# Performance work log

Hardware: AMD Instinct MI355X
Metric: run time of the kernel (lower is better)

## Reference

```python
import jax, jax.numpy as jnp
import numpy as np

DILATIONS = (1, 2, 4, 8)
K = 3  # kernel_size
B, H, W, C = 16, 128, 128, 64
HID = 256
OUT = 64  # == C, so residual path is taken


def _depthwise(x, w, dilation):
    # x: [B,H,W,C], w: [K,K,1,C] (HWIO depthwise kernel)
    pad = dilation * (K // 2)
    return jax.lax.conv_general_dilated(
        x, w,
        window_strides=(1, 1),
        padding=[(pad, pad), (pad, pad)],
        rhs_dilation=(dilation, dilation),
        dimension_numbers=('NHWC', 'HWIO', 'NHWC'),
        feature_group_count=C,
    )


def setup_inputs() -> dict:
    key = jax.random.key(0)
    k_x, k_cw, k_w1, k_b1, k_w2, k_b2 = jax.random.split(key, 6)
    in_feat = C * (1 + len(DILATIONS))  # 320
    x = jax.random.normal(k_x, (B, H, W, C), jnp.float32)
    # depthwise kernels, one [K,K,1,C] per dilation, stacked
    conv_w = jax.random.normal(k_cw, (len(DILATIONS), K, K, 1, C), jnp.float32) * (1.0 / np.sqrt(K * K).astype(np.float32))
    W1 = jax.random.normal(k_w1, (in_feat, HID), jnp.float32) * np.float32(1.0 / np.sqrt(in_feat))
    b1 = jax.random.normal(k_b1, (HID,), jnp.float32) * 0.01
    W2 = jax.random.normal(k_w2, (HID, OUT), jnp.float32) * np.float32(1.0 / np.sqrt(HID))
    b2 = jax.random.normal(k_b2, (OUT,), jnp.float32) * 0.01
    return {"x": x, "conv_w": conv_w, "W1": W1, "b1": b1, "W2": W2, "b2": b2}


def reference(x, conv_w, W1, b1, W2, b2):
    # 1) Perception: multiscale depthwise dilated convs (same-padding per dilation)
    perceptions = [_depthwise(x, conv_w[i], d) for i, d in enumerate(DILATIONS)]
    upd_in = jnp.concatenate([x] + perceptions, axis=-1)  # [B,H,W,5C]
    # 2) Update MLP: Linear -> Dropout(eval: identity) -> GELU(exact erf) -> Linear
    h = jax.nn.gelu(upd_in @ W1 + b1, approximate=False)  # [B,H,W,HID]
    delta = h @ W2 + b2  # [B,H,W,OUT]
    # 3) out_channels == channels and (eval mode or fire_rate==1.0): plain residual
    return x + delta
```

## Files before the change

### kernel.cpp

```cpp
#include <hip/hip_runtime.h>
#include <hip/hip_fp16.h>
#include <cstdint>

#define B_   16
#define H_   128
#define W_   128
#define C_   64
#define HID_ 256
#define XELEMS (B_ * H_ * W_ * C_)

typedef _Float16 __attribute__((ext_vector_type(2))) half2v;
typedef _Float16 __attribute__((ext_vector_type(8))) half8v;
typedef __attribute__((ext_vector_type(4))) float f32x4;
typedef unsigned short ushort_t;

#define W1S_OFF 0
#define W2S_OFF 81920
#define CWH_OFF 98304
#define XH_OFF  100608
#define FEAT_OFF (XH_OFF + XELEMS)
#define FEAT_HALVES (4096ull * 16384ull)
#define WS_NEED_FULL (2ull * (FEAT_OFF + FEAT_HALVES))

__device__ __forceinline__ int hs(int row, int col) {
  return row * 256 + (((col >> 3) ^ (row & 7)) << 3) + (col & 7);
}

__device__ __forceinline__ float fast_gelu(float h) {
  float u = h * fmaf(h * h, 0.10293921f, 2.30211813f);
  float e = exp2f(-u);
  return h * __builtin_amdgcn_rcpf(1.0f + e);
}

__device__ __forceinline__ uint32_t fast_gelu_pk(float h0, float h1) {
  half2v h = __builtin_bit_cast(half2v, __builtin_amdgcn_cvt_pkrtz(h0, h1));
  const half2v c1 = {(_Float16)0.10293921f, (_Float16)0.10293921f};
  const half2v c0 = {(_Float16)2.30211813f, (_Float16)2.30211813f};
  half2v u = h * (c0 + h * h * c1);
  __half2 e = h2exp2(__hneg2(__builtin_bit_cast(__half2, u)));
  const __half2 one = __half2{(__half)1.0f, (__half)1.0f};
  __half2 s = h2rcp(__hadd2(one, e));
  __half2 g = __hmul2(__builtin_bit_cast(__half2, h), s);
  return __builtin_bit_cast(uint32_t, g);
}

__device__ __forceinline__ void stage16(const _Float16* g, const ushort_t* l) {
  __builtin_amdgcn_global_load_lds(
      (const __attribute__((address_space(1))) void*)g,
      (__attribute__((address_space(3))) void*)l, 16, 0, 0);
}

__device__ __forceinline__ half2v bch(uint32_t u) {
  return __builtin_bit_cast(half2v, u);
}

__global__ void prep_kernel(const float* __restrict__ x,
                            const float* __restrict__ W1,
                            const float* __restrict__ W2,
                            const float* __restrict__ cw,
                            _Float16* __restrict__ wsb) {
  if (blockIdx.x < 393) {
    int t = blockIdx.x * 256 + threadIdx.x;
    if (t < 81920) {
      int j = t & 7, lane = (t >> 3) & 63, n16 = (t >> 9) & 15, ks = t >> 13;
      int k = ks * 32 + (lane >> 4) * 8 + j;
      int n = n16 * 16 + (lane & 15);
      wsb[W1S_OFF + t] = (_Float16)W1[k * 256 + n];
    } else if (t < 98304) {
      int t2 = t - 81920;
      int j = t2 & 7, lane = (t2 >> 3) & 63, n16 = (t2 >> 9) & 3, ks = t2 >> 11;
      int k = ks * 32 + (lane >> 4) * 8 + j;
      int n = n16 * 16 + (lane & 15);
      wsb[W2S_OFF + t2] = (_Float16)W2[k * 64 + n];
    } else if (t < 98304 + 2304) {
      int t3 = t - 98304;
      wsb[CWH_OFF + t3] = (_Float16)cw[t3];
    }
  } else {
    int i = ((blockIdx.x - 393) * 256 + threadIdx.x) * 8;
    const float4 a = *(const float4*)&x[i];
    const float4 b = *(const float4*)&x[i + 4];
    half8v o = {(_Float16)a.x, (_Float16)a.y, (_Float16)a.z, (_Float16)a.w,
                (_Float16)b.x, (_Float16)b.y, (_Float16)b.z, (_Float16)b.w};
    *(half8v*)&wsb[XH_OFF + i] = o;
  }
}

template <int DIL, int DDI>
__device__ void conv_boundary(const _Float16* __restrict__ xhb,
                              const _Float16* __restrict__ cwh,
                              _Float16* __restrict__ ft,
                              int tid, int tileX, int tileY) {
  const int quad = tid & 15;
  const int p0   = tid >> 4;
  const int ksq  = quad >> 3;
  const int c32  = (quad & 7) * 4;

  half2v w01[9], w23[9];
#pragma unroll
  for (int t = 0; t < 9; ++t) {
    uint2 wr = *(const uint2*)&cwh[(DDI * 9 + t) * C_ + quad * 4];
    w01[t] = bch(wr.x);
    w23[t] = bch(wr.y);
  }
#pragma unroll
  for (int i = 0; i < 4; ++i) {
    const int p  = i * 16 + p0;
    const int y0 = tileY + (p >> 3), x0 = tileX + (p & 7);
    half2v a01 = {0, 0}, a23 = {0, 0};
#pragma unroll
    for (int ky = 0; ky < 3; ++ky) {
      const int yy = y0 + (ky - 1) * DIL;
#pragma unroll
      for (int kx = 0; kx < 3; ++kx) {
        const int xx = x0 + (kx - 1) * DIL;
        uint2 vv = {0u, 0u};
        if ((unsigned)yy < (unsigned)H_ && (unsigned)xx < (unsigned)W_)
          vv = *(const uint2*)&xhb[(yy * W_ + xx) * C_ + quad * 4];
        const int t = ky * 3 + kx;
        a01 += bch(vv.x) * w01[t];
        a23 += bch(vv.y) * w23[t];
      }
    }
    uint2 pk;
    pk.x = __builtin_bit_cast(uint32_t, a01);
    pk.y = __builtin_bit_cast(uint32_t, a23);
    *(uint2*)&ft[(DDI * 2 + ksq) * 2048 + p * 32 + c32] = pk;
  }
}

template <int DIL, int DDI>
__global__ __launch_bounds__(256)
void conv_lds_kernel(const _Float16* __restrict__ xh,
                     const _Float16* __restrict__ cwh,
                     _Float16* __restrict__ feat) {
  constexpr int R = 8 + 2 * DIL;
  __shared__ __align__(16) ushort_t lds[R * 1024];

  const int tid   = threadIdx.x;
  const int tileX = blockIdx.x * 8;
  const int tileY = blockIdx.y * 8;
  const int batch = blockIdx.z;
  const _Float16* xhb = xh + (size_t)batch * (H_ * W_ * C_);
  _Float16* ft =
      feat + ((size_t)((batch * 16 + blockIdx.y) * 16 + blockIdx.x)) * 16384;

  const bool interior = (tileX >= 8) && (tileX <= W_ - 16) &&
                        (tileY >= 8) && (tileY <= H_ - 16);
  if (!interior) {
    conv_boundary<DIL, DDI>(xhb, cwh, ft, tid, tileX, tileY);
    return;
  }

  const int lane = tid & 63;
  const int wv   = tid >> 6;
  const int quad = tid & 15;
  const int p0   = tid >> 4;
  const int ksq  = quad >> 3;
  const int c32  = (quad & 7) * 4;

  {
    const int x0 = tileX - DIL, y0 = tileY - DIL;
    for (int s = wv; s < 2 * R; s += 4) {
      const int row = s >> 1, half = s & 1;
      const _Float16* g = &xhb[((y0 + row) * W_ + x0 + half * 8 + (lane >> 3)) * C_ +
                               (lane & 7) * 8];
      stage16(g, &lds[row * 1024 + half * 512]);
    }
  }

  half2v w01[9], w23[9];
#pragma unroll
  for (int t = 0; t < 9; ++t) {
    uint2 wr = *(const uint2*)&cwh[(DDI * 9 + t) * C_ + quad * 4];
    w01[t] = bch(wr.x);
    w23[t] = bch(wr.y);
  }

  __syncthreads();

#pragma unroll
  for (int i = 0; i < 4; ++i) {
    const int p  = i * 16 + p0;
    const int py = p >> 3, px = p & 7;
    uint2 tv[9];
#pragma unroll
    for (int ky = 0; ky < 3; ++ky)
#pragma unroll
      for (int kx = 0; kx < 3; ++kx)
        tv[ky * 3 + kx] = *(const uint2*)
            &lds[(py + ky * DIL) * 1024 + (px + kx * DIL) * 64 + quad * 4];
    half2v a01 = {0, 0}, a23 = {0, 0};
#pragma unroll
    for (int t = 0; t < 9; ++t) {
      a01 += bch(tv[t].x) * w01[t];
      a23 += bch(tv[t].y) * w23[t];
    }
    uint2 pk;
    pk.x = __builtin_bit_cast(uint32_t, a01);
    pk.y = __builtin_bit_cast(uint32_t, a23);
    *(uint2*)&ft[(DDI * 2 + ksq) * 2048 + p * 32 + c32] = pk;
  }
}

__global__ __launch_bounds__(256)
void conv_d8_kernel(const _Float16* __restrict__ xh,
                    const _Float16* __restrict__ cwh,
                    _Float16* __restrict__ feat) {
  const int tid   = threadIdx.x;
  const int tileX = blockIdx.x * 8;
  const int tileY = blockIdx.y * 8;
  const int batch = blockIdx.z;
  const _Float16* xhb = xh + (size_t)batch * (H_ * W_ * C_);
  _Float16* ft =
      feat + ((size_t)((batch * 16 + blockIdx.y) * 16 + blockIdx.x)) * 16384;

  const int c8 = tid & 7;
  const int p0 = tid >> 3;
  const int ksq = c8 >> 2;
  const int cof = (c8 & 3) * 8;

  uint4 wv4[9];
#pragma unroll
  for (int t = 0; t < 9; ++t)
    wv4[t] = *(const uint4*)&cwh[(3 * 9 + t) * C_ + c8 * 8];

  const bool interior = (tileX >= 8) && (tileX <= W_ - 16) &&
                        (tileY >= 8) && (tileY <= H_ - 16);

#pragma unroll
  for (int i = 0; i < 2; ++i) {
    const int p  = i * 32 + p0;
    const int y0 = tileY + (p >> 3), x0 = tileX + (p & 7);
    uint4 v[9];
    if (interior) {
#pragma unroll
      for (int ky = 0; ky < 3; ++ky)
#pragma unroll
        for (int kx = 0; kx < 3; ++kx)
          v[ky * 3 + kx] = *(const uint4*)
              &xhb[((y0 + (ky - 1) * 8) * W_ + x0 + (kx - 1) * 8) * C_ + c8 * 8];
    } else {
#pragma unroll
      for (int ky = 0; ky < 3; ++ky)
#pragma unroll
        for (int kx = 0; kx < 3; ++kx) {
          const int yy = y0 + (ky - 1) * 8;
          const int xx = x0 + (kx - 1) * 8;
          uint4 vv = {0u, 0u, 0u, 0u};
          if ((unsigned)yy < (unsigned)H_ && (unsigned)xx < (unsigned)W_)
            vv = *(const uint4*)&xhb[(yy * W_ + xx) * C_ + c8 * 8];
          v[ky * 3 + kx] = vv;
        }
    }
    half2v a0 = {0, 0}, a1 = {0, 0}, a2 = {0, 0}, a3 = {0, 0};
#pragma unroll
    for (int t = 0; t < 9; ++t) {
      a0 += bch(v[t].x) * bch(wv4[t].x);
      a1 += bch(v[t].y) * bch(wv4[t].y);
      a2 += bch(v[t].z) * bch(wv4[t].z);
      a3 += bch(v[t].w) * bch(wv4[t].w);
    }
    uint4 pk;
    pk.x = __builtin_bit_cast(uint32_t, a0);
    pk.y = __builtin_bit_cast(uint32_t, a1);
    pk.z = __builtin_bit_cast(uint32_t, a2);
    pk.w = __builtin_bit_cast(uint32_t, a3);
    *(uint4*)&ft[(3 * 2 + ksq) * 2048 + p * 32 + cof] = pk;
  }
}

__global__ __launch_bounds__(256, 4)
void mlp_kernel(const _Float16* __restrict__ xh,
                const _Float16* __restrict__ feat,
                const float* __restrict__ b1,
                const float* __restrict__ b2,
                const _Float16* __restrict__ w1s,
                const _Float16* __restrict__ w2s,
                float* __restrict__ out) {
  __shared__ __align__(16) ushort_t smem[64 * 256];

  const int tid   = threadIdx.x;
  const int tileX = blockIdx.x * 8;
  const int tileY = blockIdx.y * 8;
  const int batch = blockIdx.z;
  const _Float16* xhb = xh + (size_t)batch * (H_ * W_ * C_);
  const _Float16* ftb =
      feat + ((size_t)((batch * 16 + blockIdx.y) * 16 + blockIdx.x)) * 16384;

  const int lane = tid & 63;
  const int wv   = tid >> 6;
  const int lr   = lane & 15;
  const int lg   = lane >> 4;
  const int n0   = wv * 64;

  const half8v* w1v = (const half8v*)w1s;

  half8v xf[4][2];
#pragma unroll
  for (int pi = 0; pi < 4; ++pi) {
    const int p  = pi * 16 + lr;
    const int gp = (tileY + (p >> 3)) * W_ + tileX + (p & 7);
#pragma unroll
    for (int ks = 0; ks < 2; ++ks)
      xf[pi][ks] = *(const half8v*)&xhb[gp * C_ + ks * 32 + lg * 8];
  }

  {
    const _Float16* src0 = &ftb[(wv * 16 + lr) * 32 + lg * 8];
#pragma unroll
    for (int s = 0; s < 8; ++s)
      stage16(src0 + s * 2048, &smem[(s * 4 + wv) * 512]);
  }

  f32x4 acc[4][4];
#pragma unroll
  for (int hi = 0; hi < 4; ++hi)
#pragma unroll
    for (int pi = 0; pi < 4; ++pi) acc[hi][pi] = 0;

#pragma unroll
  for (int ks = 0; ks < 2; ++ks) {
    half8v wf[4];
#pragma unroll
    for (int hi = 0; hi < 4; ++hi)
      wf[hi] = w1v[(ks * 16 + wv * 4 + hi) * 64 + lane];
#pragma unroll
    for (int hi = 0; hi < 4; ++hi)
#pragma unroll
      for (int pi = 0; pi < 4; ++pi)
        acc[hi][pi] = __builtin_amdgcn_mfma_f32_16x16x32_f16(
            wf[hi], xf[pi][ks], acc[hi][pi], 0, 0, 0);
  }

  __syncthreads();

#define LOAD_W(WB, S)                                                         \
  _Pragma("unroll") for (int hi = 0; hi < 4; ++hi)                            \
      WB[hi] = w1v[((S) * 16 + wv * 4 + hi) * 64 + lane];
#define LOAD_F(FB, S)                                                         \
  _Pragma("unroll") for (int pi = 0; pi < 4; ++pi)                            \
      FB[pi] = *(const half8v*)&smem[(((S) - 2) * 4 + pi) * 512 + lane * 8];
#define MFMA16(WB, FB)                                                        \
  _Pragma("unroll") for (int hi = 0; hi < 4; ++hi)                            \
      _Pragma("unroll") for (int pi = 0; pi < 4; ++pi)                        \
      acc[hi][pi] = __builtin_amdgcn_mfma_f32_16x16x32_f16(                   \
          WB[hi], FB[pi], acc[hi][pi], 0, 0, 0);

  {
    half8v wfA[4], wfB[4], fA[4];
    LOAD_W(wfA, 2);
    LOAD_F(fA, 2); LOAD_W(wfB, 3); MFMA16(wfA, fA);
    LOAD_F(fA, 3); LOAD_W(wfA, 4); MFMA16(wfB, fA);
    LOAD_F(fA, 4); LOAD_W(wfB, 5); MFMA16(wfA, fA);
    LOAD_F(fA, 5); LOAD_W(wfA, 6); MFMA16(wfB, fA);
    LOAD_F(fA, 6); LOAD_W(wfB, 7); MFMA16(wfA, fA);
    LOAD_F(fA, 7); LOAD_W(wfA, 8); MFMA16(wfB, fA);
    LOAD_F(fA, 8); LOAD_W(wfB, 9); MFMA16(wfA, fA);
    LOAD_F(fA, 9);                 MFMA16(wfB, fA);
  }

  float4 bias1[4];
#pragma unroll
  for (int hi = 0; hi < 4; ++hi)
    bias1[hi] = *(const float4*)&b1[n0 + hi * 16 + lg * 4];

  __syncthreads();

#pragma unroll
  for (int hi = 0; hi < 4; ++hi) {
#pragma unroll
    for (int pi = 0; pi < 4; ++pi) {
      uint2 pk;
      pk.x = fast_gelu_pk(acc[hi][pi][0] + bias1[hi][0],
                          acc[hi][pi][1] + bias1[hi][1]);
      pk.y = fast_gelu_pk(acc[hi][pi][2] + bias1[hi][2],
                          acc[hi][pi][3] + bias1[hi][3]);
      *(uint2*)&smem[hs(pi * 16 + lr, n0 + hi * 16 + lg * 4)] = pk;
    }
  }
  __syncthreads();

  const int m0 = wv * 16;
  f32x4 acc2[4];
#pragma unroll
  for (int ni = 0; ni < 4; ++ni) acc2[ni] = 0;

  const half8v* w2v = (const half8v*)w2s;
#pragma unroll 2
  for (int ks = 0; ks < 8; ++ks) {
    half8v a2 = *(const half8v*)&smem[hs(m0 + lr, ks * 32 + lg * 8)];
#pragma unroll
    for (int ni = 0; ni < 4; ++ni) {
      half8v bfr = w2v[(ks * 4 + ni) * 64 + lane];
      acc2[ni] = __builtin_amdgcn_mfma_f32_16x16x32_f16(a2, bfr, acc2[ni],
                                                        0, 0, 0);
    }
  }

#pragma unroll
  for (int ni = 0; ni < 4; ++ni) {
    const int col  = ni * 16 + lr;
    const float bias = b2[col];
#pragma unroll
    for (int q = 0; q < 4; ++q) {
      const int row = m0 + lg * 4 + q;
      const int py = row >> 3, px = row & 7;
      const size_t idx =
          ((size_t)(batch * H_ + tileY + py) * W_ + (tileX + px)) * C_ + col;
      out[idx] = (float)xh[idx] + acc2[ni][q] + bias;
    }
  }
#undef LOAD_W
#undef LOAD_F
#undef MFMA16
}

template <bool BOUND>
__device__ __forceinline__ void conv_phase_f32(const float* __restrict__ xb,
                                               const _Float16* __restrict__ cwh,
                                               ushort_t* __restrict__ feat,
                                               int tid, int tileX, int tileY) {
  const int quad = tid & 15;
  const int p0   = tid >> 4;
#pragma unroll
  for (int dd = 0; dd < 4; ++dd) {
    const int dil = 1 << dd;
    half2v w01[9], w23[9];
#pragma unroll
    for (int t = 0; t < 9; ++t) {
      uint2 wr = *(const uint2*)&cwh[(dd * 9 + t) * C_ + quad * 4];
      w01[t] = bch(wr.x);
      w23[t] = bch(wr.y);
    }
#pragma unroll
    for (int i = 0; i < 4; ++i) {
      const int p  = i * 16 + p0;
      const int y0 = tileY + (p >> 3), x0 = tileX + (p & 7);
      half2v a01 = {0, 0}, a23 = {0, 0};
#pragma unroll
      for (int ky = 0; ky < 3; ++ky) {
        const int yy = y0 + (ky - 1) * dil;
        if (BOUND && (unsigned)yy >= (unsigned)H_) continue;
#pragma unroll
        for (int kx = 0; kx < 3; ++kx) {
          const int xx = x0 + (kx - 1) * dil;
          if (BOUND && (unsigned)xx >= (unsigned)W_) continue;
          const int t = ky * 3 + kx;
          const float4 xv = *(const float4*)&xb[(yy * W_ + xx) * C_ + quad * 4];
          half2v xl = {(_Float16)xv.x, (_Float16)xv.y};
          half2v xh2 = {(_Float16)xv.z, (_Float16)xv.w};
          a01 += xl * w01[t];
          a23 += xh2 * w23[t];
        }
      }
      uint2 pk;
      pk.x = __builtin_bit_cast(uint32_t, a01);
      pk.y = __builtin_bit_cast(uint32_t, a23);
      *(uint2*)&feat[hs(p, dd * 64 + quad * 4)] = pk;
    }
  }
}

__global__ __launch_bounds__(256, 4)
void nca_fused_fp32(const float* __restrict__ x,
                    const _Float16* __restrict__ cwh,
                    const float* __restrict__ b1,
                    const float* __restrict__ b2,
                    const _Float16* __restrict__ w1s,
                    const _Float16* __restrict__ w2s,
                    float* __restrict__ out) {
  __shared__ __align__(16) ushort_t smem[64 * 256];

  const int tid   = threadIdx.x;
  const int tileX = blockIdx.x * 8;
  const int tileY = blockIdx.y * 8;
  const int batch = blockIdx.z;
  const float* xb = x + (size_t)batch * (H_ * W_ * C_);

  const int lane = tid & 63;
  const int wv   = tid >> 6;
  const int lr   = lane & 15;
  const int lg   = lane >> 4;
  const int n0   = wv * 64;

  half8v xf[4][2];
#pragma unroll
  for (int pi = 0; pi < 4; ++pi) {
    const int p  = pi * 16 + lr;
    const int gp = (tileY + (p >> 3)) * W_ + tileX + (p & 7);
#pragma unroll
    for (int ks = 0; ks < 2; ++ks) {
      const float* bp = &xb[gp * C_ + ks * 32 + lg * 8];
      float4 u = *(const float4*)bp, v = *(const float4*)(bp + 4);
      half8v s = {(_Float16)u.x, (_Float16)u.y, (_Float16)u.z, (_Float16)u.w,
                  (_Float16)v.x, (_Float16)v.y, (_Float16)v.z, (_Float16)v.w};
      xf[pi][ks] = s;
    }
  }

  const bool interior = (tileX >= 8) && (tileX <= W_ - 16) &&
                        (tileY >= 8) && (tileY <= H_ - 16);
  if (interior)
    conv_phase_f32<false>(xb, cwh, smem, tid, tileX, tileY);
  else
    conv_phase_f32<true>(xb, cwh, smem, tid, tileX, tileY);
  __syncthreads();

  f32x4 acc[4][4];
#pragma unroll
  for (int hi = 0; hi < 4; ++hi)
#pragma unroll
    for (int pi = 0; pi < 4; ++pi) acc[hi][pi] = 0;

  const half8v* w1v = (const half8v*)w1s;
#pragma unroll
  for (int ks = 0; ks < 2; ++ks) {
    half8v wf[4];
#pragma unroll
    for (int hi = 0; hi < 4; ++hi)
      wf[hi] = w1v[(ks * 16 + wv * 4 + hi) * 64 + lane];
#pragma unroll
    for (int hi = 0; hi < 4; ++hi)
#pragma unroll
      for (int pi = 0; pi < 4; ++pi)
        acc[hi][pi] = __builtin_amdgcn_mfma_f32_16x16x32_f16(
            wf[hi], xf[pi][ks], acc[hi][pi], 0, 0, 0);
  }
  for (int ks = 2; ks < 10; ++ks) {
    half8v ff[4], wf[4];
#pragma unroll
    for (int pi = 0; pi < 4; ++pi)
      ff[pi] = *(const half8v*)&smem[hs(pi * 16 + lr, (ks - 2) * 32 + lg * 8)];
#pragma unroll
    for (int hi = 0; hi < 4; ++hi)
      wf[hi] = w1v[(ks * 16 + wv * 4 + hi) * 64 + lane];
#pragma unroll
    for (int hi = 0; hi < 4; ++hi)
#pragma unroll
      for (int pi = 0; pi < 4; ++pi)
        acc[hi][pi] = __builtin_amdgcn_mfma_f32_16x16x32_f16(
            wf[hi], ff[pi], acc[hi][pi], 0, 0, 0);
  }

  float4 bias1[4];
#pragma unroll
  for (int hi = 0; hi < 4; ++hi)
    bias1[hi] = *(const float4*)&b1[n0 + hi * 16 + lg * 4];

  __syncthreads();

#pragma unroll
  for (int hi = 0; hi < 4; ++hi) {
#pragma unroll
    for (int pi = 0; pi < 4; ++pi) {
      _Float16 g[4];
#pragma unroll
      for (int q = 0; q < 4; ++q)
        g[q] = (_Float16)fast_gelu(acc[hi][pi][q] + bias1[hi][q]);
      half2v g01 = {g[0], g[1]}, g23 = {g[2], g[3]};
      uint2 pk;
      pk.x = __builtin_bit_cast(uint32_t, g01);
      pk.y = __builtin_bit_cast(uint32_t, g23);
      *(uint2*)&smem[hs(pi * 16 + lr, n0 + hi * 16 + lg * 4)] = pk;
    }
  }
  __syncthreads();

  const int m0 = wv * 16;
  f32x4 acc2[4];
#pragma unroll
  for (int ni = 0; ni < 4; ++ni) acc2[ni] = 0;

  const half8v* w2v = (const half8v*)w2s;
  for (int ks = 0; ks < 8; ++ks) {
    half8v a2 = *(const half8v*)&smem[hs(m0 + lr, ks * 32 + lg * 8)];
#pragma unroll
    for (int ni = 0; ni < 4; ++ni) {
      half8v bfr = w2v[(ks * 4 + ni) * 64 + lane];
      acc2[ni] = __builtin_amdgcn_mfma_f32_16x16x32_f16(a2, bfr, acc2[ni],
                                                        0, 0, 0);
    }
  }

#pragma unroll
  for (int ni = 0; ni < 4; ++ni) {
    const int col  = ni * 16 + lr;
    const float bias = b2[col];
#pragma unroll
    for (int q = 0; q < 4; ++q) {
      const int row = m0 + lg * 4 + q;
      const int py = row >> 3, px = row & 7;
      const size_t idx =
          ((size_t)(batch * H_ + tileY + py) * W_ + (tileX + px)) * C_ + col;
      out[idx] = x[idx] + acc2[ni][q] + bias;
    }
  }
}

extern "C" void kernel_launch(void* const* d_in, const int* in_sizes, int n_in,
                              void* d_out, int out_size, void* d_ws,
                              size_t ws_size, hipStream_t stream) {
  const float* x  = (const float*)d_in[0];
  const float* cw = (const float*)d_in[1];
  const float* W1 = (const float*)d_in[2];
  const float* b1 = (const float*)d_in[3];
  const float* W2 = (const float*)d_in[4];
  const float* b2 = (const float*)d_in[5];
  float* out = (float*)d_out;

  _Float16* wsb  = (_Float16*)d_ws;
  _Float16* w1s  = wsb + W1S_OFF;
  _Float16* w2s  = wsb + W2S_OFF;
  _Float16* cwh  = wsb + CWH_OFF;
  _Float16* xh   = wsb + XH_OFF;
  _Float16* feat = wsb + FEAT_OFF;

  if (ws_size >= (size_t)WS_NEED_FULL) {
    prep_kernel<<<393 + XELEMS / 8 / 256, 256, 0, stream>>>(x, W1, W2, cw, wsb);
    dim3 g16(W_ / 8, H_ / 8, B_);
    conv_lds_kernel<1, 0><<<g16, 256, 0, stream>>>(xh, cwh, feat);
    conv_lds_kernel<2, 1><<<g16, 256, 0, stream>>>(xh, cwh, feat);
    conv_lds_kernel<4, 2><<<g16, 256, 0, stream>>>(xh, cwh, feat);
    conv_d8_kernel<<<g16, 256, 0, stream>>>(xh, cwh, feat);
    mlp_kernel<<<g16, 256, 0, stream>>>(xh, feat, b1, b2, w1s, w2s, out);
  } else {
    prep_kernel<<<393, 256, 0, stream>>>(x, W1, W2, cw, wsb);
    dim3 grid(W_ / 8, H_ / 8, B_);
    nca_fused_fp32<<<grid, 256, 0, stream>>>(x, cwh, b1, b2, w1s, w2s, out);
  }
}
```

Baseline: 198.4 us.

## Merge four per-dilation conv launches into one kernel indexed by blockIdx.z

Replaces the three templated LDS conv kernels and the separate dilation-8 kernel with one conv_all_kernel. It uses a grid four times deeper in z and picks the dilation at runtime from blockIdx.z. This removes three kernel launches and their serialization tails, so all dilations run at the same time. The dilation-8 path also issues all 18 global loads before any compute, with asm barriers to keep them grouped. In exchange, dilation becomes a runtime value rather than a compile-time constant, LDS is sized for the worst case (16 rows, 32 KB), and occupancy is bounded by launch_bounds(256,2).

After: 181.7 us, median of 2. -8.4%, faster.

```diff
diff --git a/kernel.cpp b/kernel.cpp
--- a/kernel.cpp
+++ b/kernel.cpp
@@ -86,11 +86,10 @@
   }
 }
 
-template <int DIL, int DDI>
 __device__ void conv_boundary(const _Float16* __restrict__ xhb,
                               const _Float16* __restrict__ cwh,
                               _Float16* __restrict__ ft,
-                              int tid, int tileX, int tileY) {
+                              int tid, int tileX, int tileY, int dil, int dd) {
   const int quad = tid & 15;
   const int p0   = tid >> 4;
   const int ksq  = quad >> 3;
@@ -99,7 +98,7 @@
   half2v w01[9], w23[9];
 #pragma unroll
   for (int t = 0; t < 9; ++t) {
-    uint2 wr = *(const uint2*)&cwh[(DDI * 9 + t) * C_ + quad * 4];
+    uint2 wr = *(const uint2*)&cwh[(dd * 9 + t) * C_ + quad * 4];
     w01[t] = bch(wr.x);
     w23[t] = bch(wr.y);
   }
@@ -110,10 +109,10 @@
     half2v a01 = {0, 0}, a23 = {0, 0};
 #pragma unroll
     for (int ky = 0; ky < 3; ++ky) {
-      const int yy = y0 + (ky - 1) * DIL;
+      const int yy = y0 + (ky - 1) * dil;
 #pragma unroll
       for (int kx = 0; kx < 3; ++kx) {
-        const int xx = x0 + (kx - 1) * DIL;
+        const int xx = x0 + (kx - 1) * dil;
         uint2 vv = {0u, 0u};
         if ((unsigned)yy < (unsigned)H_ && (unsigned)xx < (unsigned)W_)
           vv = *(const uint2*)&xhb[(yy * W_ + xx) * C_ + quad * 4];
@@ -125,30 +124,98 @@
     uint2 pk;
     pk.x = __builtin_bit_cast(uint32_t, a01);
     pk.y = __builtin_bit_cast(uint32_t, a23);
-    *(uint2*)&ft[(DDI * 2 + ksq) * 2048 + p * 32 + c32] = pk;
-  }
-}
-
-template <int DIL, int DDI>
-__global__ __launch_bounds__(256)
-void conv_lds_kernel(const _Float16* __restrict__ xh,
+    *(uint2*)&ft[(dd * 2 + ksq) * 2048 + p * 32 + c32] = pk;
+  }
+}
+
+__global__ __launch_bounds__(256, 2)
+void conv_all_kernel(const _Float16* __restrict__ xh,
                      const _Float16* __restrict__ cwh,
                      _Float16* __restrict__ feat) {
-  constexpr int R = 8 + 2 * DIL;
-  __shared__ __align__(16) ushort_t lds[R * 1024];
+  __shared__ __align__(16) ushort_t lds[16 * 1024];
 
   const int tid   = threadIdx.x;
   const int tileX = blockIdx.x * 8;
   const int tileY = blockIdx.y * 8;
-  const int batch = blockIdx.z;
+  const int batch = blockIdx.z >> 2;
+  const int dd    = blockIdx.z & 3;
+  const int dil   = 1 << dd;
+
   const _Float16* xhb = xh + (size_t)batch * (H_ * W_ * C_);
   _Float16* ft =
       feat + ((size_t)((batch * 16 + blockIdx.y) * 16 + blockIdx.x)) * 16384;
 
   const bool interior = (tileX >= 8) && (tileX <= W_ - 16) &&
                         (tileY >= 8) && (tileY <= H_ - 16);
+
+  if (dd == 3) {
+    const int c8 = tid & 7;
+    const int p0 = tid >> 3;
+    const int ksq = c8 >> 2;
+    const int cof = (c8 & 3) * 8;
+
+    uint4 wv4[9];
+#pragma unroll
+    for (int t = 0; t < 9; ++t)
+      wv4[t] = *(const uint4*)&cwh[(3 * 9 + t) * C_ + c8 * 8];
+
+    uint4 v[2][9];
+#pragma unroll
+    for (int i = 0; i < 2; ++i) {
+      const int p  = i * 32 + p0;
+      const int y0 = tileY + (p >> 3), x0 = tileX + (p & 7);
+      if (interior) {
+#pragma unroll
+        for (int ky = 0; ky < 3; ++ky)
+#pragma unroll
+          for (int kx = 0; kx < 3; ++kx)
+            v[i][ky * 3 + kx] = *(const uint4*)
+                &xhb[((y0 + (ky - 1) * 8) * W_ + x0 + (kx - 1) * 8) * C_ +
+                     c8 * 8];
+      } else {
+#pragma unroll
+        for (int ky = 0; ky < 3; ++ky)
+#pragma unroll
+          for (int kx = 0; kx < 3; ++kx) {
+            const int yy = y0 + (ky - 1) * 8;
+            const int xx = x0 + (kx - 1) * 8;
+            uint4 vv = {0u, 0u, 0u, 0u};
+            if ((unsigned)yy < (unsigned)H_ && (unsigned)xx < (unsigned)W_)
+              vv = *(const uint4*)&xhb[(yy * W_ + xx) * C_ + c8 * 8];
+            v[i][ky * 3 + kx] = vv;
+          }
+      }
+    }
+#pragma unroll
+    for (int i = 0; i < 2; ++i)
+#pragma unroll
+      for (int t = 0; t < 9; ++t)
+        asm volatile("" : "+v"(v[i][t].x), "+v"(v[i][t].y),
+                          "+v"(v[i][t].z), "+v"(v[i][t].w));
+
+#pragma unroll
+    for (int i = 0; i < 2; ++i) {
+      const int p = i * 32 + p0;
+      half2v a0 = {0, 0}, a1 = {0, 0}, a2 = {0, 0}, a3 = {0, 0};
+#pragma unroll
+      for (int t = 0; t < 9; ++t) {
+        a0 += bch(v[i][t].x) * bch(wv4[t].x);
+        a1 += bch(v[i][t].y) * bch(wv4[t].y);
+        a2 += bch(v[i][t].z) * bch(wv4[t].z);
+        a3 += bch(v[i][t].w) * bch(wv4[t].w);
+      }
+      uint4 pk;
+      pk.x = __builtin_bit_cast(uint32_t, a0);
+      pk.y = __builtin_bit_cast(uint32_t, a1);
+      pk.z = __builtin_bit_cast(uint32_t, a2);
+      pk.w = __builtin_bit_cast(uint32_t, a3);
+      *(uint4*)&ft[(3 * 2 + ksq) * 2048 + p * 32 + cof] = pk;
+    }
+    return;
+  }
+
   if (!interior) {
-    conv_boundary<DIL, DDI>(xhb, cwh, ft, tid, tileX, tileY);
+    conv_boundary(xhb, cwh, ft, tid, tileX, tileY, dil, dd);
     return;
   }
 
@@ -158,13 +225,15 @@
   const int p0   = tid >> 4;
   const int ksq  = quad >> 3;
   const int c32  = (quad & 7) * 4;
+  const int R    = 8 + 2 * dil;
 
   {
-    const int x0 = tileX - DIL, y0 = tileY - DIL;
+    const int x0 = tileX - dil, y0 = tileY - dil;
     for (int s = wv; s < 2 * R; s += 4) {
       const int row = s >> 1, half = s & 1;
-      const _Float16* g = &xhb[((y0 + row) * W_ + x0 + half * 8 + (lane >> 3)) * C_ +
-                               (lane & 7) * 8];
+      const _Float16* g =
+          &xhb[((y0 + row) * W_ + x0 + half * 8 + (lane >> 3)) * C_ +
+               (lane & 7) * 8];
       stage16(g, &lds[row * 1024 + half * 512]);
     }
   }
@@ -172,7 +241,7 @@
   half2v w01[9], w23[9];
 #pragma unroll
   for (int t = 0; t < 9; ++t) {
-    uint2 wr = *(const uint2*)&cwh[(DDI * 9 + t) * C_ + quad * 4];
+    uint2 wr = *(const uint2*)&cwh[(dd * 9 + t) * C_ + quad * 4];
     w01[t] = bch(wr.x);
     w23[t] = bch(wr.y);
   }
@@ -189,7 +258,7 @@
 #pragma unroll
       for (int kx = 0; kx < 3; ++kx)
         tv[ky * 3 + kx] = *(const uint2*)
-            &lds[(py + ky * DIL) * 1024 + (px + kx * DIL) * 64 + quad * 4];
+            &lds[(py + ky * dil) * 1024 + (px + kx * dil) * 64 + quad * 4];
     half2v a01 = {0, 0}, a23 = {0, 0};
 #pragma unroll
     for (int t = 0; t < 9; ++t) {
@@ -199,74 +268,7 @@
     uint2 pk;
     pk.x = __builtin_bit_cast(uint32_t, a01);
     pk.y = __builtin_bit_cast(uint32_t, a23);
-    *(uint2*)&ft[(DDI * 2 + ksq) * 2048 + p * 32 + c32] = pk;
-  }
-}
-
-__global__ __launch_bounds__(256)
-void conv_d8_kernel(const _Float16* __restrict__ xh,
-                    const _Float16* __restrict__ cwh,
-                    _Float16* __restrict__ feat) {
-  const int tid   = threadIdx.x;
-  const int tileX = blockIdx.x * 8;
-  const int tileY = blockIdx.y * 8;
-  const int batch = blockIdx.z;
-  const _Float16* xhb = xh + (size_t)batch * (H_ * W_ * C_);
-  _Float16* ft =
-      feat + ((size_t)((batch * 16 + blockIdx.y) * 16 + blockIdx.x)) * 16384;
-
-  const int c8 = tid & 7;
-  const int p0 = tid >> 3;
-  const int ksq = c8 >> 2;
-  const int cof = (c8 & 3) * 8;
-
-  uint4 wv4[9];
-#pragma unroll
-  for (int t = 0; t < 9; ++t)
-    wv4[t] = *(const uint4*)&cwh[(3 * 9 + t) * C_ + c8 * 8];
-
-  const bool interior = (tileX >= 8) && (tileX <= W_ - 16) &&
-                        (tileY >= 8) && (tileY <= H_ - 16);
-
-#pragma unroll
-  for (int i = 0; i < 2; ++i) {
-    const int p  = i * 32 + p0;
-    const int y0 = tileY + (p >> 3), x0 = tileX + (p & 7);
-    uint4 v[9];
-    if (interior) {
-#pragma unroll
-      for (int ky = 0; ky < 3; ++ky)
-#pragma unroll
-        for (int kx = 0; kx < 3; ++kx)
-          v[ky * 3 + kx] = *(const uint4*)
-              &xhb[((y0 + (ky - 1) * 8) * W_ + x0 + (kx - 1) * 8) * C_ + c8 * 8];
-    } else {
-#pragma unroll
-      for (int ky = 0; ky < 3; ++ky)
-#pragma unroll
-        for (int kx = 0; kx < 3; ++kx) {
-          const int yy = y0 + (ky - 1) * 8;
-          const int xx = x0 + (kx - 1) * 8;
-          uint4 vv = {0u, 0u, 0u, 0u};
-          if ((unsigned)yy < (unsigned)H_ && (unsigned)xx < (unsigned)W_)
-            vv = *(const uint4*)&xhb[(yy * W_ + xx) * C_ + c8 * 8];
-          v[ky * 3 + kx] = vv;
-        }
-    }
-    half2v a0 = {0, 0}, a1 = {0, 0}, a2 = {0, 0}, a3 = {0, 0};
-#pragma unroll
-    for (int t = 0; t < 9; ++t) {
-      a0 += bch(v[t].x) * bch(wv4[t].x);
-      a1 += bch(v[t].y) * bch(wv4[t].y);
-      a2 += bch(v[t].z) * bch(wv4[t].z);
-      a3 += bch(v[t].w) * bch(wv4[t].w);
-    }
-    uint4 pk;
-    pk.x = __builtin_bit_cast(uint32_t, a0);
-    pk.y = __builtin_bit_cast(uint32_t, a1);
-    pk.z = __builtin_bit_cast(uint32_t, a2);
-    pk.w = __builtin_bit_cast(uint32_t, a3);
-    *(uint4*)&ft[(3 * 2 + ksq) * 2048 + p * 32 + cof] = pk;
+    *(uint2*)&ft[(dd * 2 + ksq) * 2048 + p * 32 + c32] = pk;
   }
 }
 
@@ -618,12 +620,10 @@
 
   if (ws_size >= (size_t)WS_NEED_FULL) {
     prep_kernel<<<393 + XELEMS / 8 / 256, 256, 0, stream>>>(x, W1, W2, cw, wsb);
-    dim3 g16(W_ / 8, H_ / 8, B_);
-    conv_lds_kernel<1, 0><<<g16, 256, 0, stream>>>(xh, cwh, feat);
-    conv_lds_kernel<2, 1><<<g16, 256, 0, stream>>>(xh, cwh, feat);
-    conv_lds_kernel<4, 2><<<g16, 256, 0, stream>>>(xh, cwh, feat);
-    conv_d8_kernel<<<g16, 256, 0, stream>>>(xh, cwh, feat);
-    mlp_kernel<<<g16, 256, 0, stream>>>(xh, feat, b1, b2, w1s, w2s, out);
+    dim3 cgrid(W_ / 8, H_ / 8, B_ * 4);
+    conv_all_kernel<<<cgrid, 256, 0, stream>>>(xh, cwh, feat);
+    dim3 mgrid(W_ / 8, H_ / 8, B_);
+    mlp_kernel<<<mgrid, 256, 0, stream>>>(xh, feat, b1, b2, w1s, w2s, out);
   } else {
     prep_kernel<<<393, 256, 0, stream>>>(x, W1, W2, cw, wsb);
     dim3 grid(W_ / 8, H_ / 8, B_);
```
